# Optimization experiments

Measured on AMD Instinct MI355X. Metric: run time of the kernel, lower is better.

## Reference

```python
import jax, jax.numpy as jnp
import numpy as np

B, N, HID = 2, 2048, 1024
NH = 16
HD = HID // NH

def setup_inputs() -> dict:
    key = jax.random.key(0)
    ks = jax.random.split(key, 5)
    s = 0.02
    return {
        "hidden_states": jax.random.normal(ks[0], (B, N, HID), jnp.float32),
        "attention_mask": jnp.zeros((B, 1, 1, N), jnp.float32),
        "Wq": jax.random.normal(ks[1], (HID, HID), jnp.float32) * s,
        "bq": jnp.zeros((HID,), jnp.float32),
        "Wk": jax.random.normal(ks[2], (HID, HID), jnp.float32) * s,
        "bk": jnp.zeros((HID,), jnp.float32),
        "Wv": jax.random.normal(ks[3], (HID, HID), jnp.float32) * s,
        "bv": jnp.zeros((HID,), jnp.float32),
    }

def reference(hidden_states, attention_mask, Wq, bq, Wk, bk, Wv, bv):
    b, n, _ = hidden_states.shape
    def split_heads(t):  # [b,n,hid] -> [b,h,n,d]
        return t.reshape(b, n, NH, HD).transpose(0, 2, 1, 3)
    q = split_heads(hidden_states @ Wq.T + bq)
    k = split_heads(hidden_states @ Wk.T + bk)
    v = split_heads(hidden_states @ Wv.T + bv)
    scores = jnp.einsum('bhnd,bhmd->bhnm', q, k) / jnp.sqrt(jnp.float32(HD)).astype(q.dtype)
    scores = scores + attention_mask
    scores = jnp.maximum(scores, jnp.finfo(scores.dtype).min)
    probs = jax.nn.softmax(scores, axis=-1)
    out = jnp.einsum('bhnm,bhmd->bhnd', probs, v)
    return out.transpose(0, 2, 1, 3).reshape(b, n, NH * HD)
```

## Files before the change

kernel.cpp:

```cpp
#include <hip/hip_runtime.h>

typedef unsigned short u16;
typedef unsigned int   u32;
typedef __attribute__((ext_vector_type(8))) short bf16x8;
typedef __attribute__((ext_vector_type(4))) float f32x4;
typedef __attribute__((ext_vector_type(2))) unsigned int u32x2;

__device__ __forceinline__ float bf2f(u16 u) { return __uint_as_float(((u32)u) << 16); }
__device__ __forceinline__ u16 f2bf(float f) {
    return (u16)((__float_as_uint(f) + 0x8000u) >> 16);
}
__device__ __forceinline__ void gload16(const void* g, void* l) {
    __builtin_amdgcn_global_load_lds((const __attribute__((address_space(1))) void*)g,
                                     (__attribute__((address_space(3))) void*)l, 16, 0, 0);
}

struct us4 { u16 x, y, z, w; };
__global__ void cvt_all(const float* __restrict__ hs, const float* __restrict__ wq,
                        const float* __restrict__ wk, const float* __restrict__ wv,
                        u16* __restrict__ dst)
{
    int i = blockIdx.x * blockDim.x + threadIdx.x;
    const int stride = gridDim.x * blockDim.x;
    us4* d4 = (us4*)dst;
    for (; i < 1835008; i += stride) {
        const float4* s4;
        int j = i;
        if (j < 1048576)      { s4 = (const float4*)hs; }
        else if (j < 1310720) { s4 = (const float4*)wq; j -= 1048576; }
        else if (j < 1572864) { s4 = (const float4*)wk; j -= 1310720; }
        else                  { s4 = (const float4*)wv; j -= 1572864; }
        float4 v = s4[j];
        us4 o;
        o.x = f2bf(v.x); o.y = f2bf(v.y); o.z = f2bf(v.z); o.w = f2bf(v.w);
        d4[i] = o;
    }
}

__global__ __launch_bounds__(256) void qkv_gemm(
    const u16* __restrict__ hs,
    const u16* __restrict__ Wq, const u16* __restrict__ Wk, const u16* __restrict__ Wv,
    const float* __restrict__ bq, const float* __restrict__ bk, const float* __restrict__ bv,
    u16* __restrict__ oq, u16* __restrict__ ok, u16* __restrict__ ovt)
{
    __shared__ u16 smem[12288];
    u16* sA = smem;
    u16* sB = smem + 4096;

    const int tid  = threadIdx.x;
    const int lane = tid & 63;
    const int wv_  = tid >> 6;
    const int c15  = lane & 15;
    const int q4   = lane >> 4;
    const int rb   = blockIdx.x;
    const int mat  = blockIdx.y >> 3;
    const int cb   = blockIdx.y & 7;

    const u16*   W    = (mat == 0) ? Wq : (mat == 1 ? Wk : Wv);
    const float* bias = (mat == 0) ? bq : (mat == 1 ? bk : bv);

    f32x4 acc[4][2] = {};

    int rA[2], cA[2], rB[4], cB[4];
#pragma unroll
    for (int p = 0; p < 2; ++p) {
        const int ch = p * 256 + tid;
        rA[p] = ch >> 3; cA[p] = ((ch & 7) ^ (rA[p] & 7)) * 8;
    }
#pragma unroll
    for (int p = 0; p < 4; ++p) {
        const int ch = p * 256 + tid;
        rB[p] = ch >> 3; cB[p] = ((ch & 7) ^ (rB[p] & 7)) * 8;
    }
    const u16* gA = hs + (rb * 64) * 1024;
    const u16* gB = W + (cb * 128) * 1024;
    const int swz = c15 & 7;

    for (int kb = 0; kb < 1024; kb += 64) {
        __syncthreads();
#pragma unroll
        for (int p = 0; p < 2; ++p)
            gload16(gA + rA[p] * 1024 + kb + cA[p], sA + (p * 256 + wv_ * 64) * 8);
#pragma unroll
        for (int p = 0; p < 4; ++p)
            gload16(gB + rB[p] * 1024 + kb + cB[p], sB + (p * 256 + wv_ * 64) * 8);
        __syncthreads();

#pragma unroll
        for (int kk = 0; kk < 2; ++kk) {
            const int cpos = ((kk * 4 + q4) ^ swz) * 8;
            bf16x8 af[4], bf[2];
#pragma unroll
            for (int mt = 0; mt < 4; ++mt)
                af[mt] = *(const bf16x8*)(sA + (mt * 16 + c15) * 64 + cpos);
#pragma unroll
            for (int nt = 0; nt < 2; ++nt)
                bf[nt] = *(const bf16x8*)(sB + (wv_ * 32 + nt * 16 + c15) * 64 + cpos);
#pragma unroll
            for (int mt = 0; mt < 4; ++mt)
#pragma unroll
                for (int nt = 0; nt < 2; ++nt)
                    acc[mt][nt] = __builtin_amdgcn_mfma_f32_16x16x32_bf16(
                        af[mt], bf[nt], acc[mt][nt], 0, 0, 0);
        }
    }

    __syncthreads();
    const int hcol = cb * 2 + (wv_ >> 1);
    const int dbase = (wv_ & 1) * 32;
    float bvv[2];
#pragma unroll
    for (int nt = 0; nt < 2; ++nt)
        bvv[nt] = bias[cb * 128 + wv_ * 32 + nt * 16 + c15];

    u16* sc = smem + wv_ * 2560;
    if (mat != 2) {
        u16* dst = (mat == 0) ? oq : ok;
#pragma unroll
        for (int mt = 0; mt < 4; ++mt)
#pragma unroll
            for (int nt = 0; nt < 2; ++nt)
#pragma unroll
                for (int r = 0; r < 4; ++r)
                    sc[(mt * 16 + q4 * 4 + r) * 40 + nt * 16 + c15] =
                        f2bf(acc[mt][nt][r] + bvv[nt]);
#pragma unroll
        for (int i = 0; i < 4; ++i) {
            const int rl = i * 16 + (lane >> 2);
            const int c0 = (lane & 3) * 8;
            bf16x8 vv = *(const bf16x8*)(sc + rl * 40 + c0);
            const int n = rb * 64 + rl;
            const int bb = n >> 11, nn = n & 2047;
            *(bf16x8*)(dst + (((bb * 16 + hcol) * 2048) + nn) * 64 + dbase + c0) = vv;
        }
    } else {
#pragma unroll
        for (int mt = 0; mt < 4; ++mt)
#pragma unroll
            for (int nt = 0; nt < 2; ++nt)
#pragma unroll
                for (int r = 0; r < 4; ++r)
                    sc[(nt * 16 + c15) * 72 + mt * 16 + q4 * 4 + r] =
                        f2bf(acc[mt][nt][r] + bvv[nt]);
#pragma unroll
        for (int i = 0; i < 4; ++i) {
            const int dp = i * 8 + (lane >> 3);
            const int nl = (lane & 7) * 8;
            bf16x8 vv = *(const bf16x8*)(sc + dp * 72 + nl);
            const int n = rb * 64 + nl;
            const int bb = n >> 11, nn = n & 2047;
            *(bf16x8*)(ovt + (((bb * 16 + hcol) * 64) + dbase + dp) * 2048 + nn) = vv;
        }
    }
}

__global__ __launch_bounds__(256) void attn(
    const u16* __restrict__ qm, const u16* __restrict__ km, const u16* __restrict__ vtm,
    const float* __restrict__ mask, float* __restrict__ out)
{
    __shared__ u16 sK[64 * 64];
    __shared__ u16 sVT[64 * 64];

    const int tid = threadIdx.x, lane = tid & 63, w = tid >> 6;
    const int c15 = lane & 15, q4 = lane >> 4;
    const int qt = blockIdx.x;
    const int bh = blockIdx.y;
    const int b = bh >> 4;

    bf16x8 qf[2][2];
    const u16* qbase = qm + (bh * 2048 + qt * 128 + w * 32) * 64;
#pragma unroll
    for (int rt = 0; rt < 2; ++rt)
#pragma unroll
        for (int kt = 0; kt < 2; ++kt)
            qf[rt][kt] = *(const bf16x8*)(qbase + (rt * 16 + c15) * 64 + kt * 32 + q4 * 8);

    float l_acc[2] = {0.f, 0.f};
    f32x4 accO[2][4] = {};

    const u16* kbase  = km  + bh * 2048 * 64;
    const u16* vtbase = vtm + bh * 64 * 2048;

    const int r0 = tid >> 3,         cc0 = ((tid & 7) ^ (r0 & 7)) * 8;
    const int r1 = (256 + tid) >> 3, cc1 = ((tid & 7) ^ (r1 & 7)) * 8;

    for (int it = 0; it < 32; ++it) {
        const int kb = it * 64;
        __syncthreads();

        gload16(kbase + (kb + r0) * 64 + cc0, sK + (w * 64) * 8);
        gload16(kbase + (kb + r1) * 64 + cc1, sK + (256 + w * 64) * 8);
        gload16(vtbase + r0 * 2048 + kb + cc0, sVT + (w * 64) * 8);
        gload16(vtbase + r1 * 2048 + kb + cc1, sVT + (256 + w * 64) * 8);
        __syncthreads();

        float mkv[4][4];
#pragma unroll
        for (int ktile = 0; ktile < 4; ++ktile) {
            float4 m4 = *(const float4*)(mask + b * 2048 + kb + ktile * 16 + q4 * 4);
            mkv[ktile][0] = m4.x; mkv[ktile][1] = m4.y;
            mkv[ktile][2] = m4.z; mkv[ktile][3] = m4.w;
        }

        f32x4 accST[4][2] = {};
#pragma unroll
        for (int kt = 0; kt < 2; ++kt) {
            bf16x8 kf[4];
#pragma unroll
            for (int ktile = 0; ktile < 4; ++ktile) {
                const int key = ktile * 16 + c15;
                const int cpos = (kt * 4 + q4) ^ (key & 7);
                kf[ktile] = *(const bf16x8*)(sK + key * 64 + cpos * 8);
            }
#pragma unroll
            for (int ktile = 0; ktile < 4; ++ktile)
#pragma unroll
                for (int rt = 0; rt < 2; ++rt)
                    accST[ktile][rt] = __builtin_amdgcn_mfma_f32_16x16x32_bf16(
                        kf[ktile], qf[rt][kt], accST[ktile][rt], 0, 0, 0);
        }

        u32 pu[4][2][2];
#pragma unroll
        for (int ktile = 0; ktile < 4; ++ktile)
#pragma unroll
            for (int rt = 0; rt < 2; ++rt) {
                u32 a[4];
#pragma unroll
                for (int r = 0; r < 4; ++r) {
                    const float p = __expf(fmaf(accST[ktile][rt][r], 0.125f, mkv[ktile][r]));
                    l_acc[rt] += p;
                    a[r] = __float_as_uint(p) + 0x8000u;
                }
                pu[ktile][rt][0] = (a[0] >> 16) | (a[1] & 0xFFFF0000u);
                pu[ktile][rt][1] = (a[2] >> 16) | (a[3] & 0xFFFF0000u);
            }

#pragma unroll
        for (int g = 0; g < 2; ++g) {
            bf16x8 pA[2];
#pragma unroll
            for (int rt = 0; rt < 2; ++rt) {
                union { bf16x8 v; u32 u[4]; } t;
                t.u[0] = pu[2 * g][rt][0];
                t.u[1] = pu[2 * g][rt][1];
                t.u[2] = pu[2 * g + 1][rt][0];
                t.u[3] = pu[2 * g + 1][rt][1];
                pA[rt] = t.v;
            }
            bf16x8 vB[4];
#pragma unroll
            for (int nt = 0; nt < 4; ++nt) {
                const int d = nt * 16 + c15;
                const int pc0 = (4 * g + (q4 >> 1)) ^ (d & 7);
                const int pc1 = (4 * g + 2 + (q4 >> 1)) ^ (d & 7);
                u32x2 v0 = *(const u32x2*)(sVT + d * 64 + pc0 * 8 + (q4 & 1) * 4);
                u32x2 v1 = *(const u32x2*)(sVT + d * 64 + pc1 * 8 + (q4 & 1) * 4);
                union { bf16x8 v; u32 u[4]; } t;
                t.u[0] = v0.x; t.u[1] = v0.y; t.u[2] = v1.x; t.u[3] = v1.y;
                vB[nt] = t.v;
            }
#pragma unroll
            for (int rt = 0; rt < 2; ++rt)
#pragma unroll
                for (int nt = 0; nt < 4; ++nt)
                    accO[rt][nt] = __builtin_amdgcn_mfma_f32_16x16x32_bf16(
                        pA[rt], vB[nt], accO[rt][nt], 0, 0, 0);
        }
    }

#pragma unroll
    for (int rt = 0; rt < 2; ++rt) {
        l_acc[rt] += __shfl_xor(l_acc[rt], 16);
        l_acc[rt] += __shfl_xor(l_acc[rt], 32);
    }

    const int h = bh & 15;
#pragma unroll
    for (int rt = 0; rt < 2; ++rt) {
        float inv[4];
#pragma unroll
        for (int r = 0; r < 4; ++r)
            inv[r] = 1.0f / __shfl(l_acc[rt], q4 * 4 + r);
#pragma unroll
        for (int nt = 0; nt < 4; ++nt)
#pragma unroll
            for (int r = 0; r < 4; ++r) {
                const int qrow = qt * 128 + w * 32 + rt * 16 + q4 * 4 + r;
                const int d = nt * 16 + c15;
                out[(b * 2048 + qrow) * 1024 + h * 64 + d] = accO[rt][nt][r] * inv[r];
            }
    }
}

extern "C" void kernel_launch(void* const* d_in, const int* in_sizes, int n_in,
                              void* d_out, int out_size, void* d_ws, size_t ws_size,
                              hipStream_t stream)
{
    const float* hs   = (const float*)d_in[0];
    const float* mask = (const float*)d_in[1];
    const float* Wq   = (const float*)d_in[2];
    const float* bq   = (const float*)d_in[3];
    const float* Wk   = (const float*)d_in[4];
    const float* bk   = (const float*)d_in[5];
    const float* Wv   = (const float*)d_in[6];
    const float* bv   = (const float*)d_in[7];

    u16* ws   = (u16*)d_ws;
    u16* qw   = ws;
    u16* kw   = ws + 4194304;
    u16* vtw  = ws + 8388608;
    u16* hsb  = ws + 12582912;
    u16* wqb  = ws + 16777216;
    u16* wkb  = ws + 17825792;
    u16* wvb  = ws + 18874368;

    cvt_all<<<1024, 256, 0, stream>>>(hs, Wq, Wk, Wv, hsb);

    qkv_gemm<<<dim3(64, 24), 256, 0, stream>>>(hsb, wqb, wkb, wvb, bq, bk, bv, qw, kw, vtw);
    attn<<<dim3(16, 32), 256, 0, stream>>>(qw, kw, vtw, mask, (float*)d_out);
}
```

Baseline: 178.6 us.

## Quad-buffer K/V tiles with prefetch distance two and use exp2 softmax

Replaces the single-buffered K and V^T shared tiles with a four-slot ring. Loads for iteration it+2 are issued before computing iteration it, using a vmcnt-based waitcnt plus a single barrier instead of two __syncthreads per iteration. This is meant to hide global-to-LDS load latency behind the MFMA work. Separately, the exponential is computed with the hardware exp2 on log2e-prescaled scores and mask. The cost is four times the LDS footprint, which may reduce occupancy, plus reliance on a hand-coded waitcnt immediate; the last iterations redundantly reload tile 31.

```diff
diff --git a/kernel.cpp b/kernel.cpp
--- a/kernel.cpp
+++ b/kernel.cpp
@@ -158,8 +158,8 @@
     const u16* __restrict__ qm, const u16* __restrict__ km, const u16* __restrict__ vtm,
     const float* __restrict__ mask, float* __restrict__ out)
 {
-    __shared__ u16 sK[64 * 64];
-    __shared__ u16 sVT[64 * 64];
+    __shared__ u16 sK[4][64 * 64];
+    __shared__ u16 sVT[4][64 * 64];
 
     const int tid = threadIdx.x, lane = tid & 63, w = tid >> 6;
     const int c15 = lane & 15, q4 = lane >> 4;
@@ -184,22 +184,39 @@
     const int r0 = tid >> 3,         cc0 = ((tid & 7) ^ (r0 & 7)) * 8;
     const int r1 = (256 + tid) >> 3, cc1 = ((tid & 7) ^ (r1 & 7)) * 8;
 
+#pragma unroll
+    for (int pre = 0; pre < 2; ++pre) {
+        const int kb = pre * 64;
+        gload16(kbase + (kb + r0) * 64 + cc0, sK[pre] + (w * 64) * 8);
+        gload16(kbase + (kb + r1) * 64 + cc1, sK[pre] + (256 + w * 64) * 8);
+        gload16(vtbase + r0 * 2048 + kb + cc0, sVT[pre] + (w * 64) * 8);
+        gload16(vtbase + r1 * 2048 + kb + cc1, sVT[pre] + (256 + w * 64) * 8);
+    }
+
     for (int it = 0; it < 32; ++it) {
+        const int cur = it & 3;
+        {
+            const int itp = (it + 2 <= 31) ? (it + 2) : 31;
+            const int nb = (it + 2) & 3;
+            const int kb = itp * 64;
+            gload16(kbase + (kb + r0) * 64 + cc0, sK[nb] + (w * 64) * 8);
+            gload16(kbase + (kb + r1) * 64 + cc1, sK[nb] + (256 + w * 64) * 8);
+            gload16(vtbase + r0 * 2048 + kb + cc0, sVT[nb] + (w * 64) * 8);
+            gload16(vtbase + r1 * 2048 + kb + cc1, sVT[nb] + (256 + w * 64) * 8);
+        }
+        __builtin_amdgcn_s_waitcnt(0x0F78);
+        __builtin_amdgcn_s_barrier();
+
+        const u16* cK = sK[cur];
+        const u16* cV = sVT[cur];
         const int kb = it * 64;
-        __syncthreads();
-
-        gload16(kbase + (kb + r0) * 64 + cc0, sK + (w * 64) * 8);
-        gload16(kbase + (kb + r1) * 64 + cc1, sK + (256 + w * 64) * 8);
-        gload16(vtbase + r0 * 2048 + kb + cc0, sVT + (w * 64) * 8);
-        gload16(vtbase + r1 * 2048 + kb + cc1, sVT + (256 + w * 64) * 8);
-        __syncthreads();
 
         float mkv[4][4];
 #pragma unroll
         for (int ktile = 0; ktile < 4; ++ktile) {
             float4 m4 = *(const float4*)(mask + b * 2048 + kb + ktile * 16 + q4 * 4);
-            mkv[ktile][0] = m4.x; mkv[ktile][1] = m4.y;
-            mkv[ktile][2] = m4.z; mkv[ktile][3] = m4.w;
+            mkv[ktile][0] = m4.x * 1.44269504f; mkv[ktile][1] = m4.y * 1.44269504f;
+            mkv[ktile][2] = m4.z * 1.44269504f; mkv[ktile][3] = m4.w * 1.44269504f;
         }
 
         f32x4 accST[4][2] = {};
@@ -210,7 +227,7 @@
             for (int ktile = 0; ktile < 4; ++ktile) {
                 const int key = ktile * 16 + c15;
                 const int cpos = (kt * 4 + q4) ^ (key & 7);
-                kf[ktile] = *(const bf16x8*)(sK + key * 64 + cpos * 8);
+                kf[ktile] = *(const bf16x8*)(cK + key * 64 + cpos * 8);
             }
 #pragma unroll
             for (int ktile = 0; ktile < 4; ++ktile)
@@ -228,7 +245,8 @@
                 u32 a[4];
 #pragma unroll
                 for (int r = 0; r < 4; ++r) {
-                    const float p = __expf(fmaf(accST[ktile][rt][r], 0.125f, mkv[ktile][r]));
+                    const float p = __builtin_amdgcn_exp2f(
+                        fmaf(accST[ktile][rt][r], 0.18033688f, mkv[ktile][r]));
                     l_acc[rt] += p;
                     a[r] = __float_as_uint(p) + 0x8000u;
                 }
@@ -254,8 +272,8 @@
                 const int d = nt * 16 + c15;
                 const int pc0 = (4 * g + (q4 >> 1)) ^ (d & 7);
                 const int pc1 = (4 * g + 2 + (q4 >> 1)) ^ (d & 7);
-                u32x2 v0 = *(const u32x2*)(sVT + d * 64 + pc0 * 8 + (q4 & 1) * 4);
-                u32x2 v1 = *(const u32x2*)(sVT + d * 64 + pc1 * 8 + (q4 & 1) * 4);
+                u32x2 v0 = *(const u32x2*)(cV + d * 64 + pc0 * 8 + (q4 & 1) * 4);
+                u32x2 v1 = *(const u32x2*)(cV + d * 64 + pc1 * 8 + (q4 & 1) * 4);
                 union { bf16x8 v; u32 u[4]; } t;
                 t.u[0] = v0.x; t.u[1] = v0.y; t.u[2] = v1.x; t.u[3] = v1.y;
                 vB[nt] = t.v;
```

New measurement: 183.9 us. +2.9%, slower.
